# Optimization experiments

Hardware: AMD Instinct MI355X
Metric: run time of the kernel (lower is better)

The kernel has to match this reference:

```python
import jax, jax.numpy as jnp
import numpy as np

UNITS, ORDER, THETA, DT = 512, 256, 784.0, 1.0


def _lmu_AB(order, theta, dt):
    # Continuous-time Legendre delay system (Voelker & Eliasmith 2018)
    Q = np.arange(order, dtype=np.float64)
    R = (2.0 * Q + 1.0)[:, None] / theta
    i, j = np.meshgrid(Q, Q, indexing='ij')
    A = np.where(i < j, -1.0, (-1.0) ** (i - j + 1)) * R
    B = ((-1.0) ** Q)[:, None] * R
    # ZOH discretization: Ad = expm(A*dt); Bd = A^{-1}(Ad - I)B
    Ad = np.asarray(jax.scipy.linalg.expm(jnp.asarray(A * dt, dtype=jnp.float64)))
    Bd = np.linalg.solve(A, (Ad - np.eye(order)) @ B)
    # cell stores AT = (Ad - I)^T so that m <- m + m@AT + u@BT
    return (Ad - np.eye(order)).T.astype(np.float32), Bd.T.astype(np.float32)


def setup_inputs() -> dict:
    key = jax.random.key(0)
    ks = jax.random.split(key, 6)
    D = 1
    x = jax.random.normal(ks[0], (64, 1024, D), dtype=jnp.float32)
    # lecun_uniform: U(-sqrt(3/fan_in), sqrt(3/fan_in))
    ie = jax.random.uniform(ks[1], (D, 1), minval=-np.sqrt(3.0 / D), maxval=np.sqrt(3.0 / D), dtype=jnp.float32)
    he = jax.random.uniform(ks[2], (UNITS, 1), minval=-np.sqrt(3.0 / UNITS), maxval=np.sqrt(3.0 / UNITS), dtype=jnp.float32)
    me = jnp.zeros((ORDER, 1), dtype=jnp.float32)  # Constant(0) initializer
    # glorot_normal: std = sqrt(2/(fan_in+fan_out))
    ik = jax.random.normal(ks[3], (D, UNITS), dtype=jnp.float32) * np.sqrt(2.0 / (D + UNITS))
    hk = jax.random.normal(ks[4], (UNITS, UNITS), dtype=jnp.float32) * np.sqrt(2.0 / (2 * UNITS))
    mk = jax.random.normal(ks[5], (ORDER, UNITS), dtype=jnp.float32) * np.sqrt(2.0 / (ORDER + UNITS))
    AT, BT = _lmu_AB(ORDER, THETA / DT, DT)
    return {"x": x, "input_encoders": ie, "hidden_encoders": he, "memory_encoders": me,
            "input_kernel": ik, "hidden_kernel": hk, "memory_kernel": mk,
            "AT": jnp.asarray(AT), "BT": jnp.asarray(BT)}


def reference(x, input_encoders, hidden_encoders, memory_encoders,
              input_kernel, hidden_kernel, memory_kernel, AT, BT):
    B = x.shape[0]
    h0 = jnp.zeros((B, UNITS), dtype=x.dtype)
    m0 = jnp.zeros((B, ORDER), dtype=x.dtype)

    def step(carry, xt):  # xt: [B, D]
        h, m = carry
        u = xt @ input_encoders + h @ hidden_encoders + m @ memory_encoders  # [B,1]
        m = m + m @ AT + u @ BT                                             # [B,order]
        h = jnp.tanh(xt @ input_kernel + h @ hidden_kernel + m @ memory_kernel)
        return (h, m), h

    xs = jnp.transpose(x, (1, 0, 2))  # [T,B,D]
    _, hs = jax.lax.scan(step, (h0, m0), xs)
    return jnp.transpose(hs, (1, 0, 2))  # [B,T,units]
```

## Files before the change

### kernel.cpp

```cpp
#include <hip/hip_runtime.h>
#include <hip/hip_fp16.h>

typedef unsigned int u32;
typedef unsigned short u16;
typedef _Float16 half2v __attribute__((ext_vector_type(2)));

#define N_UNITS 512
#define N_ORDER 256
#define N_T     1024
#define N_B     64
#define KWG     4
#define PKT_STRIDE 288

__device__ inline float dot2f(u32 a, u32 b, float acc) {
    return __builtin_amdgcn_fdot2(__builtin_bit_cast(half2v, a),
                                  __builtin_bit_cast(half2v, b), acc, false);
}
__device__ inline u16 f2h_bits(float v) {
    _Float16 f = (_Float16)v;
    return __builtin_bit_cast(u16, f);
}
__device__ inline float hbits2f(u32 dw) {
    u16 s = (u16)(dw & 0xFFFFu);
    _Float16 f = __builtin_bit_cast(_Float16, s);
    return (float)f;
}
__device__ inline u32 pack_h2(float a, float b) {
    return (u32)f2h_bits(a) | ((u32)f2h_bits(b) << 16);
}
__device__ inline u32 aload(const u32* p) {
    return __hip_atomic_load(p, __ATOMIC_RELAXED, __HIP_MEMORY_SCOPE_AGENT);
}
__device__ inline void astore(u32* p, u32 v) {
    __hip_atomic_store(p, v, __ATOMIC_RELAXED, __HIP_MEMORY_SCOPE_AGENT);
}
__device__ inline float tanh_fast(float x) {
    float xa = fminf(fmaxf(x, -12.f), 12.f);
    float e  = __expf(2.f * xa);
#if __has_builtin(__builtin_amdgcn_rcpf)
    return (e - 1.f) * __builtin_amdgcn_rcpf(e + 1.f);
#else
    return (e - 1.f) / (e + 1.f);
#endif
}

__global__ __launch_bounds__(256)
void prep_hk(const float* __restrict__ hk, u32* __restrict__ hk2) {
    int tid = blockIdx.x * 256 + threadIdx.x;
    int kk = tid >> 9, c = tid & 511;
    hk2[tid] = pack_h2(hk[(2 * kk) * 512 + c], hk[(2 * kk + 1) * 512 + c]);
}

__global__ __launch_bounds__(512)
void prep_amk(const float* __restrict__ mk, const float* __restrict__ at,
              const float* __restrict__ bt,
              u32* __restrict__ amk2, float* __restrict__ bmk) {
    int bj = blockIdx.x, c = threadIdx.x;
    if (bj < 128) {
        int j0 = 2 * bj, j1 = j0 + 1;
        float a0 = mk[j0 * 512 + c];
        float a1 = mk[j1 * 512 + c];
        #pragma unroll 8
        for (int k = 0; k < 256; ++k) {
            float w = mk[k * 512 + c];
            a0 = fmaf(at[j0 * 256 + k], w, a0);
            a1 = fmaf(at[j1 * 256 + k], w, a1);
        }
        amk2[bj * 512 + c] = pack_h2(a0, a1);
    } else {
        float s = 0.f;
        #pragma unroll 8
        for (int k = 0; k < 256; ++k) s = fmaf(bt[k], mk[k * 512 + c], s);
        bmk[c] = s;
    }
}

__global__ __launch_bounds__(512, 2)
void lmu_main(const float* __restrict__ x, const float* __restrict__ ie,
              const float* __restrict__ he, const float* __restrict__ me,
              const float* __restrict__ ik, const float* __restrict__ bt,
              const float* __restrict__ at,
              const u32* __restrict__ hk2, const u32* __restrict__ amk2,
              const float* __restrict__ bmk,
              u32* __restrict__ pkt, float* __restrict__ out) {
    __shared__ float xs[N_T];
    __shared__ float he_sl[128], ik_sl[128], bmk_sl[128];
    __shared__ float me_sl[64], bt_sl[64];
    __shared__ __align__(16) u16 h_h16[N_UNITS];
    __shared__ __align__(16) u16 m_hi16[N_ORDER], m_lo16[N_ORDER];
    __shared__ __align__(16) float mf[N_ORDER];
    __shared__ __align__(16) float ufrag[12];
    __shared__ float zbuf[512], ampart[512];

    const int tid = threadIdx.x;
    const int g   = blockIdx.x;
    const int b   = g & 63;
    const int q   = g >> 6;
    const int kg  = tid >> 7;
    const int cl  = tid & 127;
    const int kg8 = tid >> 6;
    const int jl  = tid & 63;
    const int J   = 64 * q + jl;
    const int lane = tid & 63;

    for (int i = tid; i < N_T; i += 512) xs[i] = x[b * N_T + i];
    if (tid < 128) {
        he_sl[tid]  = he[128 * q + tid];
        ik_sl[tid]  = ik[128 * q + tid];
        bmk_sl[tid] = bmk[128 * q + tid];
    }
    if (tid < 64) { me_sl[tid] = me[J]; bt_sl[tid] = bt[J]; }
    h_h16[tid] = 0;
    if (tid < 256) { m_hi16[tid] = 0; m_lo16[tid] = 0; mf[tid] = 0.f; }
    if (tid < 12) ufrag[tid] = 0.f;
    const float ie0 = ie[0];

    u32 hk_w[64];
    #pragma unroll
    for (int i = 0; i < 64; ++i)
        hk_w[i] = hk2[(size_t)(64 * kg + i) * 512 + 128 * q + cl];
    u32 amk_w[32];
    #pragma unroll
    for (int i = 0; i < 32; ++i)
        amk_w[i] = amk2[(size_t)(32 * kg + i) * 512 + 128 * q + cl];
    float at_w[32];
    #pragma unroll
    for (int i = 0; i < 32; ++i)
        at_w[i] = at[(size_t)(32 * kg8 + i) * 256 + J];
    #pragma unroll
    for (int i = 0; i < 64; ++i) asm volatile("" : "+v"(hk_w[i]));
    #pragma unroll
    for (int i = 0; i < 32; ++i) asm volatile("" : "+v"(amk_w[i]));
    #pragma unroll
    for (int i = 0; i < 32; ++i) asm volatile("" : "+v"(at_w[i]));

    __syncthreads();

    const uint4*  h4   = reinterpret_cast<const uint4*>(h_h16);
    const uint4*  mh4  = reinterpret_cast<const uint4*>(m_hi16);
    const uint4*  ml4  = reinterpret_cast<const uint4*>(m_lo16);
    const float4* mfv4 = reinterpret_cast<const float4*>(mf);
    const float4* ufv4 = reinterpret_cast<const float4*>(ufrag);
    float* outb = out + (size_t)b * N_T * N_UNITS;

    float mreg = 0.f;

    for (int t = 0; t < N_T; ++t) {
        if (t > 0 && tid < 198) {
            const u32 ep  = (u32)t;
            const int par = (t - 1) & 1;
            if (tid < 192) {
                int pi = tid >> 6, i = tid & 63;
                int q2 = pi + (pi >= q ? 1 : 0);
                const u32* base = pkt + (size_t)(par * 256 + b * 4 + q2) * PKT_STRIDE;
                u32 d0, d1, d2, d3;
                if (i < 32) {
                    const u32* p4 = base + 4 * i;
                    for (;;) {
                        d0 = aload(p4 + 0); d1 = aload(p4 + 1);
                        d2 = aload(p4 + 2); d3 = aload(p4 + 3);
                        if (((((d0 >> 16) ^ ep) | ((d1 >> 16) ^ ep)) |
                             (((d2 >> 16) ^ ep) | ((d3 >> 16) ^ ep))) == 0) break;
                    }
                    int w = 32 * q2 + i;
                    *reinterpret_cast<float2*>(&mf[2 * w]) =
                        make_float2(hbits2f(d0) + hbits2f(d1),
                                    hbits2f(d2) + hbits2f(d3));
                    reinterpret_cast<u32*>(m_hi16)[w] = (d0 & 0xFFFFu) | (d2 << 16);
                    reinterpret_cast<u32*>(m_lo16)[w] = (d1 & 0xFFFFu) | (d3 << 16);
                } else {
                    const u32* p4 = base + 128 + 4 * (i - 32);
                    for (;;) {
                        d0 = aload(p4 + 0); d1 = aload(p4 + 1);
                        d2 = aload(p4 + 2); d3 = aload(p4 + 3);
                        if (((((d0 >> 16) ^ ep) | ((d1 >> 16) ^ ep)) |
                             (((d2 >> 16) ^ ep) | ((d3 >> 16) ^ ep))) == 0) break;
                    }
                    int w = 64 * q2 + 2 * (i - 32);
                    uint2 hv;
                    hv.x = (d0 & 0xFFFFu) | (d1 << 16);
                    hv.y = (d2 & 0xFFFFu) | (d3 << 16);
                    *reinterpret_cast<uint2*>(&reinterpret_cast<u32*>(h_h16)[w]) = hv;
                }
            } else {
                int r = tid - 192;
                int pi = r >> 1, sub = r & 1;
                int q2 = pi + (pi >= q ? 1 : 0);
                const u32* base =
                    pkt + (size_t)(par * 256 + b * 4 + q2) * PKT_STRIDE + 256;
                if (sub == 0) {
                    u32 d0, d1, d2, d3;
                    for (;;) {
                        d0 = aload(base + 0); d1 = aload(base + 1);
                        d2 = aload(base + 2); d3 = aload(base + 3);
                        if (((((d0 >> 16) ^ ep) | ((d1 >> 16) ^ ep)) |
                             (((d2 >> 16) ^ ep) | ((d3 >> 16) ^ ep))) == 0) break;
                    }
                    ufrag[3 * q2 + 0] = hbits2f(d0) + hbits2f(d1);
                    ufrag[3 * q2 + 1] = hbits2f(d2) + hbits2f(d3);
                } else {
                    u32 d0, d1;
                    for (;;) {
                        d0 = aload(base + 4); d1 = aload(base + 5);
                        if ((((d0 >> 16) ^ ep) | ((d1 >> 16) ^ ep)) == 0) break;
                    }
                    ufrag[3 * q2 + 2] = hbits2f(d0) + hbits2f(d1);
                }
            }
        }
        __syncthreads();

        float u;
        {
            float4 fa = ufv4[0], fb = ufv4[1], fc = ufv4[2];
            u = ((fa.x + fa.y) + (fa.z + fa.w)) + ((fb.x + fb.y) + (fb.z + fb.w))
              + ((fc.x + fc.y) + (fc.z + fc.w)) + xs[t] * ie0;
        }

        {
            float z0 = 0.f, z1 = 0.f, z2 = 0.f, z3 = 0.f;
            #pragma unroll
            for (int j = 0; j < 16; ++j) {
                uint4 hv = h4[16 * kg + j];
                z0 = dot2f(hv.x, hk_w[4 * j + 0], z0);
                z1 = dot2f(hv.y, hk_w[4 * j + 1], z1);
                z2 = dot2f(hv.z, hk_w[4 * j + 2], z2);
                z3 = dot2f(hv.w, hk_w[4 * j + 3], z3);
            }
            #pragma unroll
            for (int j = 0; j < 8; ++j) {
                uint4 mh = mh4[8 * kg + j];
                uint4 ml = ml4[8 * kg + j];
                z0 = dot2f(mh.x, amk_w[4 * j + 0], z0);
                z1 = dot2f(mh.y, amk_w[4 * j + 1], z1);
                z2 = dot2f(mh.z, amk_w[4 * j + 2], z2);
                z3 = dot2f(mh.w, amk_w[4 * j + 3], z3);
                z0 = dot2f(ml.x, amk_w[4 * j + 0], z0);
                z1 = dot2f(ml.y, amk_w[4 * j + 1], z1);
                z2 = dot2f(ml.z, amk_w[4 * j + 2], z2);
                z3 = dot2f(ml.w, amk_w[4 * j + 3], z3);
            }
            zbuf[tid] = (z0 + z1) + (z2 + z3);
            float a0 = 0.f, a1 = 0.f;
            #pragma unroll
            for (int j = 0; j < 8; ++j) {
                float4 mv = mfv4[8 * kg8 + j];
                a0 = fmaf(mv.x, at_w[4 * j + 0], a0);
                a1 = fmaf(mv.y, at_w[4 * j + 1], a1);
                a0 = fmaf(mv.z, at_w[4 * j + 2], a0);
                a1 = fmaf(mv.w, at_w[4 * j + 3], a1);
            }
            ampart[tid] = a0 + a1;
        }
        __syncthreads();

        const bool pub = (t < N_T - 1);
        const u32 eph = (u32)(t + 1) << 16;
        u32* myb = pkt + (size_t)((t & 1) * 256 + b * 4 + q) * PKT_STRIDE;

        if (tid < 128) {
            float zf = zbuf[tid] + zbuf[tid + 128] + zbuf[tid + 256] + zbuf[tid + 384]
                     + xs[t] * ik_sl[tid] + u * bmk_sl[tid];
            float hnew = tanh_fast(zf);
            u16 hb = f2h_bits(hnew);
            if (pub) astore(myb + 128 + tid, (u32)hb | eph);
            h_h16[128 * q + tid] = hb;
            outb[(size_t)t * N_UNITS + 128 * q + tid] = hnew;
            float up = hnew * he_sl[tid];
            #pragma unroll
            for (int off = 32; off > 0; off >>= 1) up += __shfl_down(up, off);
            if (lane == 0) {
                int w = tid >> 6;
                ufrag[3 * q + w] = up;
                if (pub) {
                    _Float16 hi = (_Float16)up;
                    float lo = up - (float)hi;
                    astore(myb + 256 + 2 * w,     (u32)__builtin_bit_cast(u16, hi) | eph);
                    astore(myb + 256 + 2 * w + 1, (u32)f2h_bits(lo) | eph);
                }
            }
        } else if (tid < 192) {
            float mnew = mreg + u * bt_sl[jl];
            #pragma unroll
            for (int gi = 0; gi < 8; ++gi) mnew += ampart[jl + 64 * gi];
            mreg = mnew;
            _Float16 hi = (_Float16)mnew;
            float lo = mnew - (float)hi;
            u16 hib = __builtin_bit_cast(u16, hi), lob = f2h_bits(lo);
            mf[J] = mnew;
            m_hi16[J] = hib;
            m_lo16[J] = lob;
            if (pub) {
                astore(myb + 2 * jl,     (u32)hib | eph);
                astore(myb + 2 * jl + 1, (u32)lob | eph);
            }
            float up = mnew * me_sl[jl];
            #pragma unroll
            for (int off = 32; off > 0; off >>= 1) up += __shfl_down(up, off);
            if (lane == 0) {
                ufrag[3 * q + 2] = up;
                if (pub) {
                    _Float16 uhi = (_Float16)up;
                    float ulo = up - (float)uhi;
                    astore(myb + 260, (u32)__builtin_bit_cast(u16, uhi) | eph);
                    astore(myb + 261, (u32)f2h_bits(ulo) | eph);
                }
            }
        }
    }
}

extern "C" void kernel_launch(void* const* d_in, const int* in_sizes, int n_in,
                              void* d_out, int out_size, void* d_ws, size_t ws_size,
                              hipStream_t stream) {
    const float* x  = (const float*)d_in[0];
    const float* ie = (const float*)d_in[1];
    const float* he = (const float*)d_in[2];
    const float* me = (const float*)d_in[3];
    const float* ik = (const float*)d_in[4];
    const float* hk = (const float*)d_in[5];
    const float* mk = (const float*)d_in[6];
    const float* at = (const float*)d_in[7];
    const float* bt = (const float*)d_in[8];

    u32*   hk2  = (u32*)d_ws;
    u32*   amk2 = hk2 + 256 * 512;
    float* bmk  = (float*)(amk2 + 128 * 512);
    u32*   pkt  = (u32*)(bmk + 512);

    prep_hk<<<512, 256, 0, stream>>>(hk, hk2);
    prep_amk<<<129, 512, 0, stream>>>(mk, at, bt, amk2, bmk);
    lmu_main<<<N_B * KWG, 512, 0, stream>>>(x, ie, he, me, ik, bt, at,
                                            hk2, amk2, bmk, pkt, (float*)d_out);
}
```

Baseline: 2.959 ms.

## Split each batch row across eight workgroups instead of four

Each batch element's recurrence is now split over eight cooperating workgroups (512 blocks) instead of four. Each block holds half as many hidden-kernel and memory-kernel weights in registers and does half the dot-product work per step. Peers exchange h and m slices through smaller epoch-tagged packets in global memory. The tanh reciprocal also switches to __frcp_rn. The trade-off is that every block must now poll seven peers per timestep instead of three, which adds cross-workgroup synchronization latency, and residency of all 512 blocks is needed to avoid deadlock.

```diff
diff --git a/kernel.cpp b/kernel.cpp
--- a/kernel.cpp
+++ b/kernel.cpp
@@ -9,8 +9,8 @@
 #define N_ORDER 256
 #define N_T     1024
 #define N_B     64
-#define KWG     4
-#define PKT_STRIDE 288
+#define KWG     8
+#define PKT_STRIDE 144
 
 __device__ inline float dot2f(u32 a, u32 b, float acc) {
     return __builtin_amdgcn_fdot2(__builtin_bit_cast(half2v, a),
@@ -37,11 +37,7 @@
 __device__ inline float tanh_fast(float x) {
     float xa = fminf(fmaxf(x, -12.f), 12.f);
     float e  = __expf(2.f * xa);
-#if __has_builtin(__builtin_amdgcn_rcpf)
-    return (e - 1.f) * __builtin_amdgcn_rcpf(e + 1.f);
-#else
-    return (e - 1.f) / (e + 1.f);
-#endif
+    return (e - 1.f) * __frcp_rn(e + 1.f);
 }
 
 __global__ __launch_bounds__(256)
@@ -75,7 +71,7 @@
     }
 }
 
-__global__ __launch_bounds__(512, 2)
+__global__ __launch_bounds__(512, 4)
 void lmu_main(const float* __restrict__ x, const float* __restrict__ ie,
               const float* __restrict__ he, const float* __restrict__ me,
               const float* __restrict__ ik, const float* __restrict__ bt,
@@ -84,55 +80,54 @@
               const float* __restrict__ bmk,
               u32* __restrict__ pkt, float* __restrict__ out) {
     __shared__ float xs[N_T];
-    __shared__ float he_sl[128], ik_sl[128], bmk_sl[128];
-    __shared__ float me_sl[64], bt_sl[64];
+    __shared__ float he_sl[64], ik_sl[64], bmk_sl[64];
+    __shared__ float me_sl[32], bt_sl[32];
     __shared__ __align__(16) u16 h_h16[N_UNITS];
     __shared__ __align__(16) u16 m_hi16[N_ORDER], m_lo16[N_ORDER];
     __shared__ __align__(16) float mf[N_ORDER];
-    __shared__ __align__(16) float ufrag[12];
+    __shared__ __align__(16) float ufrag[16];
     __shared__ float zbuf[512], ampart[512];
 
-    const int tid = threadIdx.x;
-    const int g   = blockIdx.x;
-    const int b   = g & 63;
-    const int q   = g >> 6;
-    const int kg  = tid >> 7;
-    const int cl  = tid & 127;
-    const int kg8 = tid >> 6;
-    const int jl  = tid & 63;
-    const int J   = 64 * q + jl;
+    const int tid  = threadIdx.x;
+    const int g    = blockIdx.x;
+    const int b    = g & 63;
+    const int q    = g >> 6;
+    const int kg   = tid >> 6;
+    const int cl   = tid & 63;
+    const int kg16 = tid >> 5;
+    const int jl2  = tid & 31;
     const int lane = tid & 63;
 
     for (int i = tid; i < N_T; i += 512) xs[i] = x[b * N_T + i];
-    if (tid < 128) {
-        he_sl[tid]  = he[128 * q + tid];
-        ik_sl[tid]  = ik[128 * q + tid];
-        bmk_sl[tid] = bmk[128 * q + tid];
+    if (tid < 64) {
+        he_sl[tid]  = he[64 * q + tid];
+        ik_sl[tid]  = ik[64 * q + tid];
+        bmk_sl[tid] = bmk[64 * q + tid];
     }
-    if (tid < 64) { me_sl[tid] = me[J]; bt_sl[tid] = bt[J]; }
+    if (tid < 32) { me_sl[tid] = me[32 * q + tid]; bt_sl[tid] = bt[32 * q + tid]; }
     h_h16[tid] = 0;
     if (tid < 256) { m_hi16[tid] = 0; m_lo16[tid] = 0; mf[tid] = 0.f; }
-    if (tid < 12) ufrag[tid] = 0.f;
+    if (tid < 16) ufrag[tid] = 0.f;
     const float ie0 = ie[0];
 
-    u32 hk_w[64];
-    #pragma unroll
-    for (int i = 0; i < 64; ++i)
-        hk_w[i] = hk2[(size_t)(64 * kg + i) * 512 + 128 * q + cl];
-    u32 amk_w[32];
+    u32 hk_w[32];
     #pragma unroll
     for (int i = 0; i < 32; ++i)
-        amk_w[i] = amk2[(size_t)(32 * kg + i) * 512 + 128 * q + cl];
-    float at_w[32];
-    #pragma unroll
-    for (int i = 0; i < 32; ++i)
-        at_w[i] = at[(size_t)(32 * kg8 + i) * 256 + J];
-    #pragma unroll
-    for (int i = 0; i < 64; ++i) asm volatile("" : "+v"(hk_w[i]));
-    #pragma unroll
-    for (int i = 0; i < 32; ++i) asm volatile("" : "+v"(amk_w[i]));
-    #pragma unroll
-    for (int i = 0; i < 32; ++i) asm volatile("" : "+v"(at_w[i]));
+        hk_w[i] = hk2[(size_t)(32 * kg + i) * 512 + 64 * q + cl];
+    u32 amk_w[16];
+    #pragma unroll
+    for (int i = 0; i < 16; ++i)
+        amk_w[i] = amk2[(size_t)(16 * kg + i) * 512 + 64 * q + cl];
+    float at_w[16];
+    #pragma unroll
+    for (int i = 0; i < 16; ++i)
+        at_w[i] = at[(size_t)(16 * kg16 + i) * 256 + 32 * q + jl2];
+    #pragma unroll
+    for (int i = 0; i < 32; ++i) asm volatile("" : "+v"(hk_w[i]));
+    #pragma unroll
+    for (int i = 0; i < 16; ++i) asm volatile("" : "+v"(amk_w[i]));
+    #pragma unroll
+    for (int i = 0; i < 16; ++i) asm volatile("" : "+v"(at_w[i]));
 
     __syncthreads();
 
@@ -146,15 +141,15 @@
     float mreg = 0.f;
 
     for (int t = 0; t < N_T; ++t) {
-        if (t > 0 && tid < 198) {
+        if (t > 0 && tid < 231) {
             const u32 ep  = (u32)t;
             const int par = (t - 1) & 1;
-            if (tid < 192) {
-                int pi = tid >> 6, i = tid & 63;
+            if (tid < 224) {
+                int pi = tid >> 5, i = tid & 31;
                 int q2 = pi + (pi >= q ? 1 : 0);
-                const u32* base = pkt + (size_t)(par * 256 + b * 4 + q2) * PKT_STRIDE;
+                const u32* base = pkt + (size_t)(par * 512 + b * 8 + q2) * PKT_STRIDE;
                 u32 d0, d1, d2, d3;
-                if (i < 32) {
+                if (i < 16) {
                     const u32* p4 = base + 4 * i;
                     for (;;) {
                         d0 = aload(p4 + 0); d1 = aload(p4 + 1);
@@ -162,75 +157,67 @@
                         if (((((d0 >> 16) ^ ep) | ((d1 >> 16) ^ ep)) |
                              (((d2 >> 16) ^ ep) | ((d3 >> 16) ^ ep))) == 0) break;
                     }
-                    int w = 32 * q2 + i;
+                    int w = 16 * q2 + i;
                     *reinterpret_cast<float2*>(&mf[2 * w]) =
                         make_float2(hbits2f(d0) + hbits2f(d1),
                                     hbits2f(d2) + hbits2f(d3));
                     reinterpret_cast<u32*>(m_hi16)[w] = (d0 & 0xFFFFu) | (d2 << 16);
                     reinterpret_cast<u32*>(m_lo16)[w] = (d1 & 0xFFFFu) | (d3 << 16);
                 } else {
-                    const u32* p4 = base + 128 + 4 * (i - 32);
+                    int j = i - 16;
+                    const u32* p4 = base + 64 + 4 * j;
                     for (;;) {
                         d0 = aload(p4 + 0); d1 = aload(p4 + 1);
                         d2 = aload(p4 + 2); d3 = aload(p4 + 3);
                         if (((((d0 >> 16) ^ ep) | ((d1 >> 16) ^ ep)) |
                              (((d2 >> 16) ^ ep) | ((d3 >> 16) ^ ep))) == 0) break;
                     }
-                    int w = 64 * q2 + 2 * (i - 32);
                     uint2 hv;
                     hv.x = (d0 & 0xFFFFu) | (d1 << 16);
                     hv.y = (d2 & 0xFFFFu) | (d3 << 16);
-                    *reinterpret_cast<uint2*>(&reinterpret_cast<u32*>(h_h16)[w]) = hv;
+                    *reinterpret_cast<uint2*>(
+                        &reinterpret_cast<u32*>(h_h16)[32 * q2 + 2 * j]) = hv;
                 }
             } else {
-                int r = tid - 192;
-                int pi = r >> 1, sub = r & 1;
-                int q2 = pi + (pi >= q ? 1 : 0);
+                int r = tid - 224;
+                int q2 = r + (r >= q ? 1 : 0);
                 const u32* base =
-                    pkt + (size_t)(par * 256 + b * 4 + q2) * PKT_STRIDE + 256;
-                if (sub == 0) {
-                    u32 d0, d1, d2, d3;
-                    for (;;) {
-                        d0 = aload(base + 0); d1 = aload(base + 1);
-                        d2 = aload(base + 2); d3 = aload(base + 3);
-                        if (((((d0 >> 16) ^ ep) | ((d1 >> 16) ^ ep)) |
-                             (((d2 >> 16) ^ ep) | ((d3 >> 16) ^ ep))) == 0) break;
-                    }
-                    ufrag[3 * q2 + 0] = hbits2f(d0) + hbits2f(d1);
-                    ufrag[3 * q2 + 1] = hbits2f(d2) + hbits2f(d3);
-                } else {
-                    u32 d0, d1;
-                    for (;;) {
-                        d0 = aload(base + 4); d1 = aload(base + 5);
-                        if ((((d0 >> 16) ^ ep) | ((d1 >> 16) ^ ep)) == 0) break;
-                    }
-                    ufrag[3 * q2 + 2] = hbits2f(d0) + hbits2f(d1);
-                }
+                    pkt + (size_t)(par * 512 + b * 8 + q2) * PKT_STRIDE + 128;
+                u32 d0, d1, d2, d3;
+                for (;;) {
+                    d0 = aload(base + 0); d1 = aload(base + 1);
+                    d2 = aload(base + 2); d3 = aload(base + 3);
+                    if (((((d0 >> 16) ^ ep) | ((d1 >> 16) ^ ep)) |
+                         (((d2 >> 16) ^ ep) | ((d3 >> 16) ^ ep))) == 0) break;
+                }
+                ufrag[2 * q2]     = hbits2f(d0) + hbits2f(d1);
+                ufrag[2 * q2 + 1] = hbits2f(d2) + hbits2f(d3);
             }
         }
         __syncthreads();
 
         float u;
         {
-            float4 fa = ufv4[0], fb = ufv4[1], fc = ufv4[2];
-            u = ((fa.x + fa.y) + (fa.z + fa.w)) + ((fb.x + fb.y) + (fb.z + fb.w))
-              + ((fc.x + fc.y) + (fc.z + fc.w)) + xs[t] * ie0;
+            float4 fa = ufv4[0], fb = ufv4[1], fc = ufv4[2], fd = ufv4[3];
+            u = (((fa.x + fa.y) + (fa.z + fa.w)) + ((fb.x + fb.y) + (fb.z + fb.w)))
+              + (((fc.x + fc.y) + (fc.z + fc.w)) + ((fd.x + fd.y) + (fd.z + fd.w)))
+              + xs[t] * ie0;
         }
 
         {
             float z0 = 0.f, z1 = 0.f, z2 = 0.f, z3 = 0.f;
             #pragma unroll
-            for (int j = 0; j < 16; ++j) {
-                uint4 hv = h4[16 * kg + j];
+            for (int j = 0; j < 8; ++j) {
+                uint4 hv = h4[8 * kg + j];
                 z0 = dot2f(hv.x, hk_w[4 * j + 0], z0);
                 z1 = dot2f(hv.y, hk_w[4 * j + 1], z1);
                 z2 = dot2f(hv.z, hk_w[4 * j + 2], z2);
                 z3 = dot2f(hv.w, hk_w[4 * j + 3], z3);
             }
             #pragma unroll
-            for (int j = 0; j < 8; ++j) {
-                uint4 mh = mh4[8 * kg + j];
-                uint4 ml = ml4[8 * kg + j];
+            for (int j = 0; j < 4; ++j) {
+                uint4 mh = mh4[4 * kg + j];
+                uint4 ml = ml4[4 * kg + j];
                 z0 = dot2f(mh.x, amk_w[4 * j + 0], z0);
                 z1 = dot2f(mh.y, amk_w[4 * j + 1], z1);
                 z2 = dot2f(mh.z, amk_w[4 * j + 2], z2);
@@ -243,8 +230,8 @@
             zbuf[tid] = (z0 + z1) + (z2 + z3);
             float a0 = 0.f, a1 = 0.f;
             #pragma unroll
-            for (int j = 0; j < 8; ++j) {
-                float4 mv = mfv4[8 * kg8 + j];
+            for (int j = 0; j < 4; ++j) {
+                float4 mv = mfv4[4 * kg16 + j];
                 a0 = fmaf(mv.x, at_w[4 * j + 0], a0);
                 a1 = fmaf(mv.y, at_w[4 * j + 1], a1);
                 a0 = fmaf(mv.z, at_w[4 * j + 2], a0);
@@ -256,54 +243,59 @@
 
         const bool pub = (t < N_T - 1);
         const u32 eph = (u32)(t + 1) << 16;
-        u32* myb = pkt + (size_t)((t & 1) * 256 + b * 4 + q) * PKT_STRIDE;
-
-        if (tid < 128) {
-            float zf = zbuf[tid] + zbuf[tid + 128] + zbuf[tid + 256] + zbuf[tid + 384]
-                     + xs[t] * ik_sl[tid] + u * bmk_sl[tid];
+        u32* myb = pkt + (size_t)((t & 1) * 512 + b * 8 + q) * PKT_STRIDE;
+
+        if (tid < 64) {
+            float zf = zbuf[tid];
+            #pragma unroll
+            for (int k = 1; k < 8; ++k) zf += zbuf[tid + 64 * k];
+            zf += xs[t] * ik_sl[tid] + u * bmk_sl[tid];
             float hnew = tanh_fast(zf);
             u16 hb = f2h_bits(hnew);
-            if (pub) astore(myb + 128 + tid, (u32)hb | eph);
-            h_h16[128 * q + tid] = hb;
-            outb[(size_t)t * N_UNITS + 128 * q + tid] = hnew;
+            if (pub) astore(myb + 64 + tid, (u32)hb | eph);
+            h_h16[64 * q + tid] = hb;
+            outb[(size_t)t * N_UNITS + 64 * q + tid] = hnew;
             float up = hnew * he_sl[tid];
             #pragma unroll
             for (int off = 32; off > 0; off >>= 1) up += __shfl_down(up, off);
             if (lane == 0) {
-                int w = tid >> 6;
-                ufrag[3 * q + w] = up;
+                ufrag[2 * q] = up;
                 if (pub) {
                     _Float16 hi = (_Float16)up;
                     float lo = up - (float)hi;
-                    astore(myb + 256 + 2 * w,     (u32)__builtin_bit_cast(u16, hi) | eph);
-                    astore(myb + 256 + 2 * w + 1, (u32)f2h_bits(lo) | eph);
-                }
-            }
-        } else if (tid < 192) {
-            float mnew = mreg + u * bt_sl[jl];
-            #pragma unroll
-            for (int gi = 0; gi < 8; ++gi) mnew += ampart[jl + 64 * gi];
-            mreg = mnew;
-            _Float16 hi = (_Float16)mnew;
-            float lo = mnew - (float)hi;
-            u16 hib = __builtin_bit_cast(u16, hi), lob = f2h_bits(lo);
-            mf[J] = mnew;
-            m_hi16[J] = hib;
-            m_lo16[J] = lob;
-            if (pub) {
-                astore(myb + 2 * jl,     (u32)hib | eph);
-                astore(myb + 2 * jl + 1, (u32)lob | eph);
-            }
-            float up = mnew * me_sl[jl];
+                    astore(myb + 128, (u32)__builtin_bit_cast(u16, hi) | eph);
+                    astore(myb + 129, (u32)f2h_bits(lo) | eph);
+                }
+            }
+        } else if (tid < 128) {
+            int jl = tid - 64;
+            float up = 0.f;
+            if (jl < 32) {
+                float mnew = mreg + u * bt_sl[jl];
+                #pragma unroll
+                for (int gi = 0; gi < 16; ++gi) mnew += ampart[jl + 32 * gi];
+                mreg = mnew;
+                _Float16 hi = (_Float16)mnew;
+                float lo = mnew - (float)hi;
+                u16 hib = __builtin_bit_cast(u16, hi), lob = f2h_bits(lo);
+                mf[32 * q + jl] = mnew;
+                m_hi16[32 * q + jl] = hib;
+                m_lo16[32 * q + jl] = lob;
+                if (pub) {
+                    astore(myb + 2 * jl,     (u32)hib | eph);
+                    astore(myb + 2 * jl + 1, (u32)lob | eph);
+                }
+                up = mnew * me_sl[jl];
+            }
             #pragma unroll
             for (int off = 32; off > 0; off >>= 1) up += __shfl_down(up, off);
             if (lane == 0) {
-                ufrag[3 * q + 2] = up;
+                ufrag[2 * q + 1] = up;
                 if (pub) {
                     _Float16 uhi = (_Float16)up;
                     float ulo = up - (float)uhi;
-                    astore(myb + 260, (u32)__builtin_bit_cast(u16, uhi) | eph);
-                    astore(myb + 261, (u32)f2h_bits(ulo) | eph);
+                    astore(myb + 130, (u32)__builtin_bit_cast(u16, uhi) | eph);
+                    astore(myb + 131, (u32)f2h_bits(ulo) | eph);
                 }
             }
         }
```

Result: slower. 6.713 ms (+126.9%).
